# Kernel tuning notes

Hardware: AMD Instinct MI355X
Metric: run time of the kernel (lower is better)

The kernel has to match this reference:

```python
import jax, jax.numpy as jnp
import numpy as np

N = 50000      # graph nodes
E = 400000     # random edges (plus N self-loops)
F = 128        # graph feature dim
H = 4          # GAT heads (layer1)
DH = 64        # gnn_hidden_size (per-head out, layer1)
EMB = 8        # emb_size / GAT final out
B = 16384      # batch
NS = 20        # number of sparse features
V = 1000       # vocab per sparse feature
DENSE = 64     # num_fea_size
HID = 256      # hidden_dims
EPS = 1e-5


def setup_inputs():
    key = jax.random.key(0)
    ks = jax.random.split(key, 40)
    loop = jnp.arange(N, dtype=jnp.int32)
    src = jnp.concatenate([jax.random.randint(ks[0], (E,), 0, N, dtype=jnp.int32), loop])
    dst = jnp.concatenate([jax.random.randint(ks[1], (E,), 0, N, dtype=jnp.int32), loop])
    s = 0.05
    d = {
        'X_id': jax.random.randint(ks[2], (B, 2), 0, N),
        'X_sparse': jax.random.randint(ks[3], (B, NS), 0, V),
        'X_dense': jax.random.normal(ks[4], (B, DENSE), jnp.float32),
        'emb_tables': jax.random.normal(ks[5], (NS, V, EMB), jnp.float32) * s,
        'graph_feature': jax.random.normal(ks[6], (N, F), jnp.float32),
        'src': src, 'dst': dst,
        'wide_w': jax.random.normal(ks[7], (EMB, DENSE), jnp.float32) * s,
        'wide_b': jnp.zeros((EMB,), jnp.float32),
        'lin1_w': jax.random.normal(ks[8], (HID, NS * EMB + DENSE), jnp.float32) * s,
        'lin1_b': jnp.zeros((HID,), jnp.float32),
        'bn1_g': jnp.ones((HID,), jnp.float32),
        'bn1_b': jnp.zeros((HID,), jnp.float32),
        'bn1_m': jax.random.normal(ks[9], (HID,), jnp.float32) * s,
        'bn1_v': jnp.ones((HID,), jnp.float32),
        'lin2_w': jax.random.normal(ks[10], (HID, HID), jnp.float32) * s,
        'lin2_b': jnp.zeros((HID,), jnp.float32),
        'bn2_g': jnp.ones((HID,), jnp.float32),
        'bn2_b': jnp.zeros((HID,), jnp.float32),
        'bn2_m': jax.random.normal(ks[11], (HID,), jnp.float32) * s,
        'bn2_v': jnp.ones((HID,), jnp.float32),
        'dnn_w': jax.random.normal(ks[12], (EMB, HID), jnp.float32) * s,
        'dnn_b': jnp.zeros((EMB,), jnp.float32),
        'gat1_w': jax.random.normal(ks[13], (H * DH, F), jnp.float32) * s,
        'gat1_al': jax.random.normal(ks[14], (H, DH), jnp.float32) * s,
        'gat1_ar': jax.random.normal(ks[15], (H, DH), jnp.float32) * s,
        'gat1_bias': jnp.zeros((H * DH,), jnp.float32),
        'gat2_w': jax.random.normal(ks[16], (EMB, H * DH), jnp.float32) * s,
        'gat2_al': jax.random.normal(ks[17], (1, EMB), jnp.float32) * s,
        'gat2_ar': jax.random.normal(ks[18], (1, EMB), jnp.float32) * s,
        'gat2_bias': jnp.zeros((EMB,), jnp.float32),
        'g1w': jax.random.normal(ks[19], (1, EMB), jnp.float32) * s,
        'g1b': jnp.zeros((1,), jnp.float32),
        'g2w': jax.random.normal(ks[20], (1, EMB), jnp.float32) * s,
        'g2b': jnp.zeros((1,), jnp.float32),
        'g3w': jax.random.normal(ks[21], (1, EMB), jnp.float32) * s,
        'g3b': jnp.zeros((1,), jnp.float32),
        'gout_w': jax.random.normal(ks[22], (2, 3 * EMB), jnp.float32) * s,
        'gout_b': jnp.zeros((2,), jnp.float32),
    }
    return d


def gat_conv(h, W, al, ar, bias, src, dst, heads, dh):
    # DGL GATConv: project, per-edge attention, edge-softmax over dst, aggregate
    feat = (h @ W.T).reshape(-1, heads, dh)          # [N, H, D]
    el = (feat * al).sum(-1)                          # [N, H] src score
    er = (feat * ar).sum(-1)                          # [N, H] dst score
    e = jax.nn.leaky_relu(el[src] + er[dst], 0.2)     # [Etot, H]
    emax = jax.lax.stop_gradient(jax.ops.segment_max(e, dst, num_segments=N))
    a = jnp.exp(e - emax[dst])
    denom = jax.ops.segment_sum(a, dst, num_segments=N)  # [N, H]
    alpha = a / denom[dst]                            # [Etot, H]
    out = jax.ops.segment_sum(alpha[:, :, None] * feat[src], dst, num_segments=N)
    return out + bias.reshape(1, heads, dh)           # [N, H, D]


def batchnorm_eval(x, g, b, m, v):
    return g * (x - m) * jax.lax.rsqrt(v + EPS) + b


def reference(X_id, X_sparse, X_dense, emb_tables, graph_feature, src, dst,
              wide_w, wide_b, lin1_w, lin1_b, bn1_g, bn1_b, bn1_m, bn1_v,
              lin2_w, lin2_b, bn2_g, bn2_b, bn2_m, bn2_v, dnn_w, dnn_b,
              gat1_w, gat1_al, gat1_ar, gat1_bias, gat2_w, gat2_al, gat2_ar, gat2_bias,
              g1w, g1b, g2w, g2b, g3w, g3b, gout_w, gout_b):
    commit_ids = X_id[:, 1]
    # sparse embedding lookup: [B, NS, EMB] -> [B, NS*EMB]
    sparse_embed = emb_tables[jnp.arange(NS)[None, :], X_sparse].reshape(B, NS * EMB)
    x = jnp.concatenate([sparse_embed, X_dense], axis=-1)
    wide_out = X_dense @ wide_w.T + wide_b            # [B, EMB]
    # deep MLP (eval-mode BN, dropout = identity)
    d = jax.nn.relu(batchnorm_eval(x @ lin1_w.T + lin1_b, bn1_g, bn1_b, bn1_m, bn1_v))
    d = jax.nn.relu(batchnorm_eval(d @ lin2_w.T + lin2_b, bn2_g, bn2_b, bn2_m, bn2_v))
    deep_out = d @ dnn_w.T + dnn_b                    # [B, EMB]
    # GAT
    h1 = gat_conv(graph_feature, gat1_w, gat1_al, gat1_ar, gat1_bias, src, dst, H, DH)
    h1 = jax.nn.elu(h1.reshape(N, H * DH))
    h2 = gat_conv(h1, gat2_w, gat2_al, gat2_ar, gat2_bias, src, dst, 1, EMB)
    gcn = h2.reshape(N, EMB)                          # squeeze head dim
    gcn_out = gcn[commit_ids]                         # [B, EMB]
    # Gate (concat)
    aw = jax.nn.sigmoid(wide_out @ g1w.T + g1b)
    bw = jax.nn.sigmoid(deep_out @ g2w.T + g2b)
    cw = jax.nn.sigmoid(gcn_out @ g3w.T + g3b)
    tot = aw + bw + cw
    combined = jnp.concatenate([(aw / tot) * wide_out, (bw / tot) * deep_out,
                                (cw / tot) * gcn_out], axis=1)
    out = combined @ gout_w.T + gout_b                # [B, 2]
    return jax.nn.softmax(out, axis=1)
```

## Files before the change

kernel.cpp:

```cpp
#include <hip/hip_runtime.h>

#define TPB 256
constexpr float BN_EPS = 1e-5f;

typedef __attribute__((ext_vector_type(8))) short short8;
typedef __attribute__((ext_vector_type(4))) float floatx4;

__device__ __forceinline__ float sigmoidf_(float x) { return 1.f / (1.f + __expf(-x)); }
__device__ __forceinline__ unsigned short f2bf(float f) {
    unsigned u = __float_as_uint(f);
    u += 0x7FFFu + ((u >> 16) & 1u);
    return (unsigned short)(u >> 16);
}
__device__ __forceinline__ float bf2f(unsigned short h) {
    return __uint_as_float((unsigned)h << 16);
}

__global__ __launch_bounds__(TPB) void prep_kernel(
    const float* __restrict__ w1, unsigned short* __restrict__ o1,
    const float* __restrict__ w2, unsigned short* __restrict__ o2,
    const float* __restrict__ w3, unsigned short* __restrict__ o3,
    const float* __restrict__ gfeat, unsigned short* __restrict__ gfeatb, int ng4,
    const int* __restrict__ Xs, const float* __restrict__ Xd,
    const float* __restrict__ emb, unsigned short* __restrict__ x, int nx, int B)
{
    const int NW = 256 * 224 + 256 * 256 + 256 * 128;
    int idx = blockIdx.x * TPB + threadIdx.x;
    if (idx < NW) {
        if (idx < 256 * 224) o1[idx] = f2bf(w1[idx]);
        else if (idx < 256 * 224 + 256 * 256) o2[idx - 256 * 224] = f2bf(w2[idx - 256 * 224]);
        else o3[idx - 256 * 224 - 256 * 256] = f2bf(w3[idx - 256 * 224 - 256 * 256]);
        return;
    }
    int i = idx - NW;
    if (i < ng4) {
        float4 v = ((const float4*)gfeat)[i];
        ushort4 o;
        o.x = f2bf(v.x); o.y = f2bf(v.y); o.z = f2bf(v.z); o.w = f2bf(v.w);
        ((ushort4*)gfeatb)[i] = o;
        return;
    }
    i -= ng4;
    if (i >= nx) return;
    int b = i / 224, c = i - b * 224;
    float v;
    if (c < 160) {
        int s = c >> 3, j = c & 7;
        int e = Xs[b * 20 + s];
        v = emb[((size_t)s * 1000 + e) * 8 + j];
    } else {
        v = Xd[b * 64 + (c - 160)];
    }
    x[i] = f2bf(v);
}

template<bool BNRELU>
__global__ __launch_bounds__(256) void gemm_mfma(
    const unsigned short* __restrict__ A, const unsigned short* __restrict__ W,
    const float* __restrict__ bias,
    const float* __restrict__ g, const float* __restrict__ bb,
    const float* __restrict__ bm, const float* __restrict__ bv,
    unsigned short* __restrict__ C, int M, int N, int K)
{
    constexpr int SK = 40;
    __shared__ unsigned short As[64 * SK];
    __shared__ unsigned short Bs[64 * SK];
    int tid = threadIdx.x;
    int wave = tid >> 6, lane = tid & 63;
    int wm = (wave & 1) * 32, wn = (wave >> 1) * 32;
    int m0 = blockIdx.x * 64, n0 = blockIdx.y * 64;
    int lrow = lane & 15, lk = (lane >> 4) * 8;
    floatx4 acc[2][2] = {};
    for (int k0 = 0; k0 < K; k0 += 32) {
        {
            int r = tid >> 2, seg = (tid & 3) * 8;
            uint4 av = make_uint4(0u, 0u, 0u, 0u);
            int gm = m0 + r;
            if (gm < M) av = *(const uint4*)(A + (size_t)gm * K + k0 + seg);
            *(uint4*)(As + r * SK + seg) = av;
            uint4 wv = make_uint4(0u, 0u, 0u, 0u);
            int gn = n0 + r;
            if (gn < N) wv = *(const uint4*)(W + (size_t)gn * K + k0 + seg);
            *(uint4*)(Bs + r * SK + seg) = wv;
        }
        __syncthreads();
        short8 af[2], bfr[2];
#pragma unroll
        for (int i = 0; i < 2; ++i)
            af[i] = *(const short8*)(As + (wm + i * 16 + lrow) * SK + lk);
#pragma unroll
        for (int j = 0; j < 2; ++j)
            bfr[j] = *(const short8*)(Bs + (wn + j * 16 + lrow) * SK + lk);
#pragma unroll
        for (int i = 0; i < 2; ++i)
#pragma unroll
            for (int j = 0; j < 2; ++j)
                acc[i][j] = __builtin_amdgcn_mfma_f32_16x16x32_bf16(
                    af[i], bfr[j], acc[i][j], 0, 0, 0);
        __syncthreads();
    }
    int crow = (lane >> 4) * 4, ccol = lane & 15;
#pragma unroll
    for (int j = 0; j < 2; ++j) {
        int gn = n0 + wn + j * 16 + ccol;
        float sc = 1.f, sh = 0.f;
        if (BNRELU) {
            sc = g[gn] * rsqrtf(bv[gn] + BN_EPS);
            sh = (bias[gn] - bm[gn]) * sc + bb[gn];
        }
#pragma unroll
        for (int i = 0; i < 2; ++i) {
#pragma unroll
            for (int r = 0; r < 2 * 2; ++r) {
                int gm = m0 + wm + i * 16 + crow + r;
                if (gm >= M) continue;
                float t = acc[i][j][r];
                if (BNRELU) t = fmaxf(t * sc + sh, 0.f);
                C[(size_t)gm * N + gn] = f2bf(t);
            }
        }
    }
}

__global__ __launch_bounds__(TPB) void heads_kernel(
    const float* __restrict__ Xd, const float* __restrict__ Ww,
    const float* __restrict__ wb, float* __restrict__ wide,
    const unsigned short* __restrict__ d2, const float* __restrict__ Wd,
    const float* __restrict__ db, float* __restrict__ deep, int B)
{
    int nb = (B + 3) / 4;
    int lane = threadIdx.x & 63;
    float p[8];
    if ((int)blockIdx.x < nb) {
        int r = blockIdx.x * 4 + (threadIdx.x >> 6);
        if (r >= B) return;
        float a = Xd[(size_t)r * 64 + lane];
#pragma unroll
        for (int j = 0; j < 8; ++j) p[j] = a * Ww[j * 64 + lane];
#pragma unroll
        for (int off = 1; off < 64; off <<= 1)
#pragma unroll
            for (int j = 0; j < 8; ++j) p[j] += __shfl_xor(p[j], off, 64);
        if (lane == 0) {
#pragma unroll
            for (int j = 0; j < 8; ++j) wide[(size_t)r * 8 + j] = p[j] + wb[j];
        }
    } else {
        int r = (blockIdx.x - nb) * 4 + (threadIdx.x >> 6);
        if (r >= B) return;
        uint2 ab = *(const uint2*)(d2 + (size_t)r * 256 + lane * 4);
        float a0 = bf2f((unsigned short)(ab.x & 0xFFFFu));
        float a1 = bf2f((unsigned short)(ab.x >> 16));
        float a2 = bf2f((unsigned short)(ab.y & 0xFFFFu));
        float a3 = bf2f((unsigned short)(ab.y >> 16));
#pragma unroll
        for (int j = 0; j < 8; ++j) {
            float4 wv = *(const float4*)(Wd + j * 256 + lane * 4);
            p[j] = a0 * wv.x + a1 * wv.y + a2 * wv.z + a3 * wv.w;
        }
#pragma unroll
        for (int off = 1; off < 64; off <<= 1)
#pragma unroll
            for (int j = 0; j < 8; ++j) p[j] += __shfl_xor(p[j], off, 64);
        if (lane == 0) {
#pragma unroll
            for (int j = 0; j < 8; ++j) deep[(size_t)r * 8 + j] = p[j] + db[j];
        }
    }
}

template<int HN, int DHD>
__global__ __launch_bounds__(TPB) void attn_coef_bf16(
    const unsigned short* __restrict__ feat, const float* __restrict__ al,
    const float* __restrict__ ar, float* __restrict__ el, float* __restrict__ er, int Nn)
{
    int idx = blockIdx.x * TPB + threadIdx.x;
    if (idx >= Nn * HN) return;
    int n = idx / HN, h = idx - n * HN;
    const uint2* f4 = (const uint2*)(feat + (size_t)n * (HN * DHD) + h * DHD);
    const float4* al4 = (const float4*)(al + h * DHD);
    const float4* ar4 = (const float4*)(ar + h * DHD);
    float sl = 0.f, sr = 0.f;
#pragma unroll
    for (int d = 0; d < DHD / 4; ++d) {
        uint2 fb = f4[d];
        float f0 = bf2f((unsigned short)(fb.x & 0xFFFFu));
        float f1 = bf2f((unsigned short)(fb.x >> 16));
        float f2 = bf2f((unsigned short)(fb.y & 0xFFFFu));
        float f3 = bf2f((unsigned short)(fb.y >> 16));
        float4 lv = al4[d], rv = ar4[d];
        sl += f0 * lv.x + f1 * lv.y + f2 * lv.z + f3 * lv.w;
        sr += f0 * rv.x + f1 * rv.y + f2 * rv.z + f3 * rv.w;
    }
    el[idx] = sl; er[idx] = sr;
}

__global__ __launch_bounds__(TPB) void hist_kernel(
    const int* __restrict__ dst, int* __restrict__ cnt, int E)
{
    int i = blockIdx.x * TPB + threadIdx.x;
    if (i >= E) return;
    atomicAdd(&cnt[dst[i]], 1);
}

__global__ __launch_bounds__(256) void scan_local(
    const int* __restrict__ cnt, int* __restrict__ rowstart,
    int* __restrict__ blocksum, int Nn)
{
    __shared__ int wsum[4];
    int tid = threadIdx.x;
    int lane = tid & 63, wid = tid >> 6;
    int base = blockIdx.x * 1024 + tid * 4;
    int v0 = (base + 0 < Nn) ? cnt[base + 0] : 0;
    int v1 = (base + 1 < Nn) ? cnt[base + 1] : 0;
    int v2 = (base + 2 < Nn) ? cnt[base + 2] : 0;
    int v3 = (base + 3 < Nn) ? cnt[base + 3] : 0;
    int s1 = v0 + v1, s2 = s1 + v2, s3 = s2 + v3;
    int v = s3;
#pragma unroll
    for (int off = 1; off < 64; off <<= 1) {
        int t = __shfl_up(v, off, 64);
        if (lane >= off) v += t;
    }
    if (lane == 63) wsum[wid] = v;
    __syncthreads();
    int woff = 0;
#pragma unroll
    for (int w = 0; w < 4; ++w) woff += (w < wid) ? wsum[w] : 0;
    int excl = woff + v - s3;
    if (base + 0 < Nn) rowstart[base + 1] = excl + v0;
    if (base + 1 < Nn) rowstart[base + 2] = excl + s1;
    if (base + 2 < Nn) rowstart[base + 3] = excl + s2;
    if (base + 3 < Nn) rowstart[base + 4] = excl + s3;
    if (tid == 255) blocksum[blockIdx.x] = woff + v;
}

__global__ __launch_bounds__(64) void scan_blocks(
    const int* __restrict__ blocksum, int* __restrict__ blockoff, int nblocks)
{
    int lane = threadIdx.x;
    int v = (lane < nblocks) ? blocksum[lane] : 0;
#pragma unroll
    for (int off = 1; off < 64; off <<= 1) {
        int t = __shfl_up(v, off, 64);
        if (lane >= off) v += t;
    }
    if (lane < nblocks) blockoff[lane] = v - blocksum[lane];
}

__global__ __launch_bounds__(TPB) void add_offsets(
    int* __restrict__ rowstart, const int* __restrict__ blockoff,
    int* __restrict__ cursor, int Nn)
{
    int i = blockIdx.x * TPB + threadIdx.x;
    if (i >= Nn) return;
    int v = rowstart[i + 1] + blockoff[i >> 10];
    rowstart[i + 1] = v;
    if (i + 1 < Nn) cursor[i + 1] = v;
    if (i == 0) { rowstart[0] = 0; cursor[0] = 0; }
}

__global__ __launch_bounds__(TPB) void scatter_kernel(
    const int* __restrict__ src, const int* __restrict__ dst,
    int* __restrict__ cursor, int* __restrict__ esrc, int E)
{
    int i = blockIdx.x * TPB + threadIdx.x;
    if (i >= E) return;
    int pos = atomicAdd(&cursor[dst[i]], 1);
    esrc[pos] = src[i];
}

__global__ __launch_bounds__(TPB) void gat1_gather_fused(
    const unsigned short* __restrict__ feat, const float* __restrict__ el,
    const float* __restrict__ er, const int* __restrict__ rowstart,
    const int* __restrict__ esrc, const float* __restrict__ bias,
    const float* __restrict__ w2, const float* __restrict__ al2,
    const float* __restrict__ ar2,
    float* __restrict__ feat2, float* __restrict__ el2, float* __restrict__ er2, int Nn)
{
    int n = blockIdx.x * 4 + (threadIdx.x >> 6);
    if (n >= Nn) return;
    int lane = threadIdx.x & 63;
    int h = lane >> 4;
    int c = h * 64 + (lane & 15) * 4;
    float erv = er[n * 4 + h];
    int beg = rowstart[n], end = rowstart[n + 1];
    float4 acc = make_float4(0.f, 0.f, 0.f, 0.f);
    float dsum = 0.f;
    int e = beg;
    for (; e + 4 <= end; e += 4) {
        int sv[4]; float lv[4]; uint2 fb[4];
#pragma unroll
        for (int u = 0; u < 4; ++u) sv[u] = esrc[e + u];
#pragma unroll
        for (int u = 0; u < 4; ++u) lv[u] = el[sv[u] * 4 + h];
#pragma unroll
        for (int u = 0; u < 4; ++u) fb[u] = *(const uint2*)(feat + (size_t)sv[u] * 256 + c);
#pragma unroll
        for (int u = 0; u < 4; ++u) {
            float ev = lv[u] + erv;
            ev = ev > 0.f ? ev : 0.2f * ev;
            float av = __expf(ev);
            dsum += av;
            acc.x += av * bf2f((unsigned short)(fb[u].x & 0xFFFFu));
            acc.y += av * bf2f((unsigned short)(fb[u].x >> 16));
            acc.z += av * bf2f((unsigned short)(fb[u].y & 0xFFFFu));
            acc.w += av * bf2f((unsigned short)(fb[u].y >> 16));
        }
    }
    for (; e < end; ++e) {
        int s = esrc[e];
        float ev = el[s * 4 + h] + erv;
        ev = ev > 0.f ? ev : 0.2f * ev;
        float av = __expf(ev);
        dsum += av;
        uint2 fb = *(const uint2*)(feat + (size_t)s * 256 + c);
        acc.x += av * bf2f((unsigned short)(fb.x & 0xFFFFu));
        acc.y += av * bf2f((unsigned short)(fb.x >> 16));
        acc.z += av * bf2f((unsigned short)(fb.y & 0xFFFFu));
        acc.w += av * bf2f((unsigned short)(fb.y >> 16));
    }
    float inv = 1.f / dsum;
    float4 bv = *(const float4*)(bias + c);
    float4 o;
    o.x = acc.x * inv + bv.x; o.y = acc.y * inv + bv.y;
    o.z = acc.z * inv + bv.z; o.w = acc.w * inv + bv.w;
    o.x = o.x > 0.f ? o.x : __expf(o.x) - 1.f;
    o.y = o.y > 0.f ? o.y : __expf(o.y) - 1.f;
    o.z = o.z > 0.f ? o.z : __expf(o.z) - 1.f;
    o.w = o.w > 0.f ? o.w : __expf(o.w) - 1.f;
    float p[8];
#pragma unroll
    for (int j = 0; j < 8; ++j) {
        float4 wv = *(const float4*)(w2 + j * 256 + c);
        p[j] = o.x * wv.x + o.y * wv.y + o.z * wv.z + o.w * wv.w;
    }
#pragma unroll
    for (int off = 1; off < 64; off <<= 1)
#pragma unroll
        for (int j = 0; j < 8; ++j)
            p[j] += __shfl_xor(p[j], off, 64);
    if (lane == 0) {
        float e_l = 0.f, e_r = 0.f;
#pragma unroll
        for (int j = 0; j < 8; ++j) {
            feat2[(size_t)n * 8 + j] = p[j];
            e_l += p[j] * al2[j];
            e_r += p[j] * ar2[j];
        }
        el2[n] = e_l; er2[n] = e_r;
    }
}

__global__ __launch_bounds__(TPB) void gat2_gather_b(
    const float* __restrict__ feat2, const float* __restrict__ el,
    const float* __restrict__ er, const int* __restrict__ rowstart,
    const int* __restrict__ esrc, const int* __restrict__ Xid,
    float* __restrict__ gcn, int B)
{
    int idx = blockIdx.x * TPB + threadIdx.x;
    if (idx >= B * 8) return;
    int b = idx >> 3, j = idx & 7;
    int n = Xid[b * 2 + 1];
    float erv = er[n];
    int beg = rowstart[n], end = rowstart[n + 1];
    float acc = 0.f, dsum = 0.f;
    int e = beg;
    for (; e + 4 <= end; e += 4) {
        int sv[4]; float lv[4], fv[4];
#pragma unroll
        for (int u = 0; u < 4; ++u) sv[u] = esrc[e + u];
#pragma unroll
        for (int u = 0; u < 4; ++u) lv[u] = el[sv[u]];
#pragma unroll
        for (int u = 0; u < 4; ++u) fv[u] = feat2[(size_t)sv[u] * 8 + j];
#pragma unroll
        for (int u = 0; u < 4; ++u) {
            float ev = lv[u] + erv;
            ev = ev > 0.f ? ev : 0.2f * ev;
            float av = __expf(ev);
            dsum += av;
            acc += av * fv[u];
        }
    }
    for (; e < end; ++e) {
        int s = esrc[e];
        float ev = el[s] + erv;
        ev = ev > 0.f ? ev : 0.2f * ev;
        float av = __expf(ev);
        dsum += av;
        acc += av * feat2[(size_t)s * 8 + j];
    }
    gcn[idx] = acc / dsum;
}

__global__ __launch_bounds__(TPB) void final_kernel(
    const float* __restrict__ wide, const float* __restrict__ deep,
    const float* __restrict__ gcn,
    const float* __restrict__ g2bias,
    const float* __restrict__ g1w, const float* __restrict__ g1b,
    const float* __restrict__ g2w, const float* __restrict__ g2b,
    const float* __restrict__ g3w, const float* __restrict__ g3b,
    const float* __restrict__ goutw, const float* __restrict__ goutb,
    float* __restrict__ out, int B)
{
    int b = blockIdx.x * TPB + threadIdx.x;
    if (b >= B) return;
    float w8[8], d8[8], g8[8];
    {
        float4 t0 = *(const float4*)(wide + (size_t)b * 8);
        float4 t1 = *(const float4*)(wide + (size_t)b * 8 + 4);
        w8[0] = t0.x; w8[1] = t0.y; w8[2] = t0.z; w8[3] = t0.w;
        w8[4] = t1.x; w8[5] = t1.y; w8[6] = t1.z; w8[7] = t1.w;
        t0 = *(const float4*)(deep + (size_t)b * 8);
        t1 = *(const float4*)(deep + (size_t)b * 8 + 4);
        d8[0] = t0.x; d8[1] = t0.y; d8[2] = t0.z; d8[3] = t0.w;
        d8[4] = t1.x; d8[5] = t1.y; d8[6] = t1.z; d8[7] = t1.w;
        t0 = *(const float4*)(gcn + (size_t)b * 8);
        t1 = *(const float4*)(gcn + (size_t)b * 8 + 4);
        g8[0] = t0.x; g8[1] = t0.y; g8[2] = t0.z; g8[3] = t0.w;
        g8[4] = t1.x; g8[5] = t1.y; g8[6] = t1.z; g8[7] = t1.w;
    }
#pragma unroll
    for (int j = 0; j < 8; ++j) g8[j] += g2bias[j];
    float s1 = g1b[0], s2 = g2b[0], s3 = g3b[0];
#pragma unroll
    for (int j = 0; j < 8; ++j) { s1 += w8[j] * g1w[j]; s2 += d8[j] * g2w[j]; s3 += g8[j] * g3w[j]; }
    float aw = sigmoidf_(s1), bw = sigmoidf_(s2), cw = sigmoidf_(s3);
    float inv_tot = 1.f / (aw + bw + cw);
    float an = aw * inv_tot, bn = bw * inv_tot, cn = cw * inv_tot;
    float o0 = goutb[0], o1 = goutb[1];
#pragma unroll
    for (int j = 0; j < 8; ++j) {
        float c0 = an * w8[j]; o0 += goutw[j] * c0;      o1 += goutw[24 + j] * c0;
        float c1 = bn * d8[j]; o0 += goutw[8 + j] * c1;  o1 += goutw[32 + j] * c1;
        float c2 = cn * g8[j]; o0 += goutw[16 + j] * c2; o1 += goutw[40 + j] * c2;
    }
    float mx = fmaxf(o0, o1);
    float e0 = __expf(o0 - mx), e1 = __expf(o1 - mx);
    float inv = 1.f / (e0 + e1);
    out[(size_t)b * 2] = e0 * inv;
    out[(size_t)b * 2 + 1] = e1 * inv;
}

extern "C" void kernel_launch(void* const* d_in, const int* in_sizes, int n_in,
                              void* d_out, int out_size, void* d_ws, size_t ws_size,
                              hipStream_t stream)
{
    const int*   Xid    = (const int*)d_in[0];
    const int*   Xs     = (const int*)d_in[1];
    const float* Xd     = (const float*)d_in[2];
    const float* emb    = (const float*)d_in[3];
    const float* gfeat  = (const float*)d_in[4];
    const int*   src    = (const int*)d_in[5];
    const int*   dst    = (const int*)d_in[6];
    const float* wide_w = (const float*)d_in[7];
    const float* wide_b = (const float*)d_in[8];
    const float* lin1_w = (const float*)d_in[9];
    const float* lin1_b = (const float*)d_in[10];
    const float* bn1_g  = (const float*)d_in[11];
    const float* bn1_b  = (const float*)d_in[12];
    const float* bn1_m  = (const float*)d_in[13];
    const float* bn1_v  = (const float*)d_in[14];
    const float* lin2_w = (const float*)d_in[15];
    const float* lin2_b = (const float*)d_in[16];
    const float* bn2_g  = (const float*)d_in[17];
    const float* bn2_b  = (const float*)d_in[18];
    const float* bn2_m  = (const float*)d_in[19];
    const float* bn2_v  = (const float*)d_in[20];
    const float* dnn_w  = (const float*)d_in[21];
    const float* dnn_b  = (const float*)d_in[22];
    const float* gat1_w = (const float*)d_in[23];
    const float* gat1_al = (const float*)d_in[24];
    const float* gat1_ar = (const float*)d_in[25];
    const float* gat1_bias = (const float*)d_in[26];
    const float* gat2_w = (const float*)d_in[27];
    const float* gat2_al = (const float*)d_in[28];
    const float* gat2_ar = (const float*)d_in[29];
    const float* gat2_bias = (const float*)d_in[30];
    const float* g1w = (const float*)d_in[31];
    const float* g1b = (const float*)d_in[32];
    const float* g2w = (const float*)d_in[33];
    const float* g2b = (const float*)d_in[34];
    const float* g3w = (const float*)d_in[35];
    const float* g3b = (const float*)d_in[36];
    const float* goutw = (const float*)d_in[37];
    const float* goutb = (const float*)d_in[38];

    const int B    = in_sizes[0] / 2;
    const int Nn   = in_sizes[4] / 128;
    const int Etot = in_sizes[5];

    char* base = (char*)d_ws;
    size_t off = 0;
    auto alloc = [&](size_t bytes) -> char* {
        char* p = base + off;
        off += (bytes + 255) & ~(size_t)255;
        return p;
    };
    unsigned short* xb = (unsigned short*)alloc((size_t)B * 224 * 2);
    unsigned short* d1 = (unsigned short*)alloc((size_t)B * 256 * 2);
    unsigned short* d2 = (unsigned short*)alloc((size_t)B * 256 * 2);
    unsigned short* feat1  = (unsigned short*)alloc((size_t)Nn * 256 * 2);
    unsigned short* gfeatb = (unsigned short*)alloc((size_t)Nn * 128 * 2);
    unsigned short* w1b = (unsigned short*)alloc(256 * 224 * 2);
    unsigned short* w2b = (unsigned short*)alloc(256 * 256 * 2);
    unsigned short* wg1b = (unsigned short*)alloc(256 * 128 * 2);
    float* wide  = (float*)alloc((size_t)B * 8 * 4);
    float* deep  = (float*)alloc((size_t)B * 8 * 4);
    float* el1   = (float*)alloc((size_t)Nn * 4 * 4);
    float* er1   = (float*)alloc((size_t)Nn * 4 * 4);
    float* feat2 = (float*)alloc((size_t)Nn * 8 * 4);
    float* el2   = (float*)alloc((size_t)Nn * 4);
    float* er2   = (float*)alloc((size_t)Nn * 4);
    float* gcn   = (float*)alloc((size_t)B * 8 * 4);
    int* rowstart = (int*)alloc((size_t)(Nn + 1) * 4);
    int* cnt      = (int*)alloc((size_t)(Nn + 1) * 4);
    int* cursor   = (int*)alloc((size_t)Nn * 4);
    int* esrc     = (int*)alloc((size_t)Etot * 4);
    int* blocksum = (int*)alloc(64 * 4);
    int* blockoff = (int*)alloc(64 * 4);

    const int nScanBlocks = (Nn + 1023) / 1024;

    hipMemsetAsync(cnt, 0, (size_t)(Nn + 1) * sizeof(int), stream);
    hist_kernel<<<(Etot + TPB - 1) / TPB, TPB, 0, stream>>>(dst, cnt, Etot);
    scan_local<<<nScanBlocks, 256, 0, stream>>>(cnt, rowstart, blocksum, Nn);
    scan_blocks<<<1, 64, 0, stream>>>(blocksum, blockoff, nScanBlocks);
    add_offsets<<<(Nn + TPB - 1) / TPB, TPB, 0, stream>>>(rowstart, blockoff, cursor, Nn);
    scatter_kernel<<<(Etot + TPB - 1) / TPB, TPB, 0, stream>>>(src, dst, cursor, esrc, Etot);

    {
        const int NW = 256 * 224 + 256 * 256 + 256 * 128;
        const int NG4 = Nn * 128 / 4;
        const int NX = B * 224;
        int total = NW + NG4 + NX;
        prep_kernel<<<(total + TPB - 1) / TPB, TPB, 0, stream>>>(
            lin1_w, w1b, lin2_w, w2b, gat1_w, wg1b,
            gfeat, gfeatb, NG4, Xs, Xd, emb, xb, NX, B);
    }

    gemm_mfma<true><<<dim3((B + 63) / 64, 4), 256, 0, stream>>>(
        xb, w1b, lin1_b, bn1_g, bn1_b, bn1_m, bn1_v, d1, B, 256, 224);
    gemm_mfma<true><<<dim3((B + 63) / 64, 4), 256, 0, stream>>>(
        d1, w2b, lin2_b, bn2_g, bn2_b, bn2_m, bn2_v, d2, B, 256, 256);
    heads_kernel<<<2 * ((B + 3) / 4), TPB, 0, stream>>>(
        Xd, wide_w, wide_b, wide, d2, dnn_w, dnn_b, deep, B);

    gemm_mfma<false><<<dim3((Nn + 63) / 64, 4), 256, 0, stream>>>(
        gfeatb, wg1b, nullptr, nullptr, nullptr, nullptr, nullptr, feat1, Nn, 256, 128);
    attn_coef_bf16<4, 64><<<(Nn * 4 + TPB - 1) / TPB, TPB, 0, stream>>>(
        feat1, gat1_al, gat1_ar, el1, er1, Nn);
    gat1_gather_fused<<<(Nn + 3) / 4, TPB, 0, stream>>>(
        feat1, el1, er1, rowstart, esrc, gat1_bias,
        gat2_w, gat2_al, gat2_ar, feat2, el2, er2, Nn);

    gat2_gather_b<<<(B * 8 + TPB - 1) / TPB, TPB, 0, stream>>>(
        feat2, el2, er2, rowstart, esrc, Xid, gcn, B);

    final_kernel<<<(B + TPB - 1) / TPB, TPB, 0, stream>>>(
        wide, deep, gcn, gat2_bias, g1w, g1b, g2w, g2b, g3w, g3b, goutw, goutb,
        (float*)d_out, B);
}
```

Baseline: 338.7 us.

## Prefetch GEMM tiles into registers with K=64 steps and unroll GAT gather by 8

The MFMA GEMM now steps K in 64-wide tiles and keeps the next tile's global loads in registers while the current tile is computed from shared memory. This overlaps global memory latency with MFMA work and halves the barrier count. The first GAT aggregation kernel gets an 8-way unrolled edge loop so more gathers are in flight at once. Both changes raise register and LDS use, which may lower occupancy.

After: 407.2 us. 20.2% more time.

```diff
diff --git a/kernel.cpp b/kernel.cpp
--- a/kernel.cpp
+++ b/kernel.cpp
@@ -62,7 +62,7 @@
     const float* __restrict__ bm, const float* __restrict__ bv,
     unsigned short* __restrict__ C, int M, int N, int K)
 {
-    constexpr int SK = 40;
+    constexpr int SK = 72;
     __shared__ unsigned short As[64 * SK];
     __shared__ unsigned short Bs[64 * SK];
     int tid = threadIdx.x;
@@ -71,32 +71,54 @@
     int m0 = blockIdx.x * 64, n0 = blockIdx.y * 64;
     int lrow = lane & 15, lk = (lane >> 4) * 8;
     floatx4 acc[2][2] = {};
-    for (int k0 = 0; k0 < K; k0 += 32) {
-        {
-            int r = tid >> 2, seg = (tid & 3) * 8;
-            uint4 av = make_uint4(0u, 0u, 0u, 0u);
-            int gm = m0 + r;
-            if (gm < M) av = *(const uint4*)(A + (size_t)gm * K + k0 + seg);
-            *(uint4*)(As + r * SK + seg) = av;
-            uint4 wv = make_uint4(0u, 0u, 0u, 0u);
-            int gn = n0 + r;
-            if (gn < N) wv = *(const uint4*)(W + (size_t)gn * K + k0 + seg);
-            *(uint4*)(Bs + r * SK + seg) = wv;
+    const int nk = (K + 63) >> 6;
+    uint4 ra[2], rb[2];
+#pragma unroll
+    for (int i = 0; i < 2; ++i) {
+        int idx = tid + i * 256;
+        int r = idx >> 3, seg = (idx & 7) * 8;
+        uint4 z = make_uint4(0u, 0u, 0u, 0u);
+        ra[i] = (m0 + r < M && seg < K) ? *(const uint4*)(A + (size_t)(m0 + r) * K + seg) : z;
+        rb[i] = (n0 + r < N && seg < K) ? *(const uint4*)(W + (size_t)(n0 + r) * K + seg) : z;
+    }
+    for (int kt = 0; kt < nk; ++kt) {
+#pragma unroll
+        for (int i = 0; i < 2; ++i) {
+            int idx = tid + i * 256;
+            int r = idx >> 3, seg = (idx & 7) * 8;
+            *(uint4*)(As + r * SK + seg) = ra[i];
+            *(uint4*)(Bs + r * SK + seg) = rb[i];
         }
         __syncthreads();
-        short8 af[2], bfr[2];
-#pragma unroll
-        for (int i = 0; i < 2; ++i)
-            af[i] = *(const short8*)(As + (wm + i * 16 + lrow) * SK + lk);
-#pragma unroll
-        for (int j = 0; j < 2; ++j)
-            bfr[j] = *(const short8*)(Bs + (wn + j * 16 + lrow) * SK + lk);
-#pragma unroll
-        for (int i = 0; i < 2; ++i)
+        if (kt + 1 < nk) {
+            int k0 = (kt + 1) * 64;
+#pragma unroll
+            for (int i = 0; i < 2; ++i) {
+                int idx = tid + i * 256;
+                int r = idx >> 3, seg = (idx & 7) * 8;
+                uint4 z = make_uint4(0u, 0u, 0u, 0u);
+                ra[i] = (m0 + r < M && k0 + seg < K)
+                          ? *(const uint4*)(A + (size_t)(m0 + r) * K + k0 + seg) : z;
+                rb[i] = (n0 + r < N && k0 + seg < K)
+                          ? *(const uint4*)(W + (size_t)(n0 + r) * K + k0 + seg) : z;
+            }
+        }
+#pragma unroll
+        for (int kk = 0; kk < 2; ++kk) {
+            short8 af[2], bfr[2];
+#pragma unroll
+            for (int i = 0; i < 2; ++i)
+                af[i] = *(const short8*)(As + (wm + i * 16 + lrow) * SK + kk * 32 + lk);
 #pragma unroll
             for (int j = 0; j < 2; ++j)
-                acc[i][j] = __builtin_amdgcn_mfma_f32_16x16x32_bf16(
-                    af[i], bfr[j], acc[i][j], 0, 0, 0);
+                bfr[j] = *(const short8*)(Bs + (wn + j * 16 + lrow) * SK + kk * 32 + lk);
+#pragma unroll
+            for (int i = 0; i < 2; ++i)
+#pragma unroll
+                for (int j = 0; j < 2; ++j)
+                    acc[i][j] = __builtin_amdgcn_mfma_f32_16x16x32_bf16(
+                        af[i], bfr[j], acc[i][j], 0, 0, 0);
+        }
         __syncthreads();
     }
     int crow = (lane >> 4) * 4, ccol = lane & 15;
@@ -111,7 +133,7 @@
 #pragma unroll
         for (int i = 0; i < 2; ++i) {
 #pragma unroll
-            for (int r = 0; r < 2 * 2; ++r) {
+            for (int r = 0; r < 4; ++r) {
                 int gm = m0 + wm + i * 16 + crow + r;
                 if (gm >= M) continue;
                 float t = acc[i][j][r];
@@ -288,6 +310,26 @@
     float4 acc = make_float4(0.f, 0.f, 0.f, 0.f);
     float dsum = 0.f;
     int e = beg;
+    for (; e + 8 <= end; e += 8) {
+        int sv[8]; float lv[8]; uint2 fb[8];
+#pragma unroll
+        for (int u = 0; u < 8; ++u) sv[u] = esrc[e + u];
+#pragma unroll
+        for (int u = 0; u < 8; ++u) lv[u] = el[sv[u] * 4 + h];
+#pragma unroll
+        for (int u = 0; u < 8; ++u) fb[u] = *(const uint2*)(feat + (size_t)sv[u] * 256 + c);
+#pragma unroll
+        for (int u = 0; u < 8; ++u) {
+            float ev = lv[u] + erv;
+            ev = ev > 0.f ? ev : 0.2f * ev;
+            float av = __expf(ev);
+            dsum += av;
+            acc.x += av * bf2f((unsigned short)(fb[u].x & 0xFFFFu));
+            acc.y += av * bf2f((unsigned short)(fb[u].x >> 16));
+            acc.z += av * bf2f((unsigned short)(fb[u].y & 0xFFFFu));
+            acc.w += av * bf2f((unsigned short)(fb[u].y >> 16));
+        }
+    }
     for (; e + 4 <= end; e += 4) {
         int sv[4]; float lv[4]; uint2 fb[4];
 #pragma unroll
```
